# Kernel optimization log

Hardware: AMD Instinct MI355X
Metric: run time of the kernel (lower is better)

Reference implementation:

```python
import jax, jax.numpy as jnp
from jax import lax
import numpy as np

GRID = 64
HIDDEN = 256
FEAT = 128


def setup_inputs() -> dict:
    key = jax.random.key(0)
    ks = jax.random.split(key, 16)
    B, S = 1024, 4096
    def w(k, shape, fan_in):
        return (jax.random.normal(k, shape, jnp.float32) * (1.0 / np.sqrt(fan_in))).astype(jnp.float32)
    return {
        "x": jax.random.normal(ks[0], (B, 2, S), jnp.float32),
        # conv stack
        "w1": w(ks[1], (32, 1, 3, 3), 9),    "b1": jnp.zeros((32,), jnp.float32),  "a1": jnp.float32(0.25),
        "w2": w(ks[2], (64, 32, 3, 3), 32 * 9),  "b2": jnp.zeros((64,), jnp.float32),  "a2": jnp.float32(0.25),
        "w3": w(ks[3], (128, 64, 5, 5), 64 * 25), "b3": jnp.zeros((128,), jnp.float32), "a3": jnp.float32(0.25),
        # classifier (dropout is identity in eval mode)
        "wc1": w(ks[4], (HIDDEN, 128 * 4 * 4), 128 * 16), "bc1": jnp.zeros((HIDDEN,), jnp.float32), "ac": jnp.float32(0.25),
        "wc2": w(ks[5], (FEAT, HIDDEN), HIDDEN),          "bc2": jnp.zeros((FEAT,), jnp.float32),
    }


def _prelu(x, a):
    return jnp.where(x > 0, x, a * x)


def _conv(x, w, b, pad):
    y = lax.conv_general_dilated(x, w, (1, 1), [(pad, pad), (pad, pad)],
                                 dimension_numbers=("NCHW", "OIHW", "NCHW"))
    return y + b[None, :, None, None]


def _avgpool2(x):  # kernel 2, stride 2 (also serves as adaptive pool 8->4)
    B, C, H, W = x.shape
    return x.reshape(B, C, H // 2, 2, W // 2, 2).mean(axis=(3, 5))


def _iq_to_constellation(x):
    # x: [B, 2, S] -> occupancy grid [B, 1, G, G] (set to 1.0, duplicates collapse)
    B = x.shape[0]
    scale = GRID // 2 / 2.0
    offset = GRID // 2
    ii = jnp.clip((x[:, 0] * scale + offset).astype(jnp.int32), 0, GRID - 1)  # [B,S]
    qi = jnp.clip((x[:, 1] * scale + offset).astype(jnp.int32), 0, GRID - 1)
    img = jnp.zeros((B, 1, GRID, GRID), x.dtype)
    bidx = jnp.arange(B)[:, None]
    return img.at[bidx, 0, qi, ii].set(1.0)


def reference(x, w1, b1, a1, w2, b2, a2, w3, b3, a3, wc1, bc1, ac, wc2, bc2):
    img = _iq_to_constellation(x)                      # [B,1,64,64]
    h = _avgpool2(_prelu(_conv(img, w1, b1, 1), a1))   # [B,32,32,32]
    h = _avgpool2(_prelu(_conv(h, w2, b2, 1), a2))     # [B,64,16,16]
    h = _avgpool2(_prelu(_conv(h, w3, b3, 2), a3))     # [B,128,8,8]
    h = _avgpool2(h)                                   # adaptive 8x8 -> 4x4
    h = h.reshape(h.shape[0], -1)                      # [B, 2048]
    h = _prelu(h @ wc1.T + bc1, ac)                    # [B, 256]
    return h @ wc2.T + bc2                             # [B, 128]
```

## Files before the change

kernel.cpp:

```cpp
#include <hip/hip_runtime.h>


typedef short s16x8 __attribute__((ext_vector_type(8)));
typedef float f32x4 __attribute__((ext_vector_type(4)));
typedef float f32x16 __attribute__((ext_vector_type(16)));
typedef unsigned u32x4 __attribute__((ext_vector_type(4)));
typedef unsigned u32x2 __attribute__((ext_vector_type(2)));

__device__ __forceinline__ float prelu(float v, float a) {
    return v > 0.0f ? v : a * v;
}
__device__ __forceinline__ unsigned short bf16_rn(float x) {
    union { float f; unsigned u; } a; a.f = x;
    unsigned r = a.u + 0x7FFF + ((a.u >> 16) & 1);
    return (unsigned short)(r >> 16);
}
__device__ __forceinline__ unsigned pack2(float lo, float hi) {
    return (unsigned)bf16_rn(lo) | ((unsigned)bf16_rn(hi) << 16);
}

__global__ __launch_bounds__(256) void k_prepack_all(
    const float* __restrict__ w3, unsigned short* __restrict__ w3pk,
    const float* __restrict__ w2, unsigned short* __restrict__ w2pk,
    const float* __restrict__ wc1, unsigned short* __restrict__ wf1pk,
    const float* __restrict__ wc2, unsigned short* __restrict__ wf2pk)
{
    const int bid = blockIdx.x;
    const int t = threadIdx.x;
    if (bid < 800) {
        int e = bid * 256 + t;
        int i  = e & 7;
        int co = (e >> 3) & 127;
        int g  = (e >> 10) & 3;
        int kk = (e >> 12) & 1;
        int tp = e >> 13;
        int ci = kk * 32 + g * 8 + i;
        w3pk[e] = bf16_rn(w3[((size_t)co * 64 + ci) * 25 + tp]);
    } else if (bid < 872) {
        int e = (bid - 800) * 256 + t;
        int i   = e & 7;
        int l   = (e >> 3) & 63;
        int mt  = (e >> 9) & 1;
        int kkk = (e >> 10) & 1;
        int tap = e >> 11;
        int co = mt * 32 + (l & 31);
        int ci = kkk * 16 + (l >> 5) * 8 + i;
        w2pk[e] = bf16_rn(w2[((size_t)co * 32 + ci) * 9 + tap]);
    } else if (bid < 2920) {
        int e = (bid - 872) * 256 + t;
        int i   = e & 7;
        int hid = (e >> 3) & 255;
        int g   = (e >> 11) & 3;
        int kc  = e >> 13;
        int k = kc * 32 + g * 8 + i;
        wf1pk[e] = bf16_rn(wc1[(size_t)hid * 2048 + k]);
    } else {
        int e = (bid - 2920) * 256 + t;
        int i  = e & 7;
        int o  = (e >> 3) & 127;
        int g  = (e >> 10) & 3;
        int kc = e >> 12;
        int k = kc * 32 + g * 8 + i;
        wf2pk[e] = bf16_rn(wc2[(size_t)o * 256 + k]);
    }
}

__global__ __launch_bounds__(256) void k_scat_conv1(
    const float* __restrict__ x, const float* __restrict__ w1,
    const float* __restrict__ b1, const float* __restrict__ a1,
    unsigned short* __restrict__ out1, int b0)
{
    __shared__ float img[34 * 66];
    __shared__ float ws[32 * 9];
    __shared__ float bs[32];
    const int t = threadIdx.x;
    const int bl = blockIdx.x >> 1;
    const int yb = blockIdx.x & 1;
    const int b = b0 + bl;

    for (int i = t; i < 34 * 66; i += 256) img[i] = 0.0f;
    for (int i = t; i < 288; i += 256) ws[i] = w1[i];
    if (t < 32) bs[t] = b1[t];
    __syncthreads();

    const float* xb = x + (size_t)b * 8192;
    const int rbase = yb * 32 - 1;
    for (int s = t; s < 4096; s += 256) {
        float xi = xb[s];
        float xq = xb[4096 + s];
        int ii = (int)(xi * 16.0f + 32.0f);
        int qi = (int)(xq * 16.0f + 32.0f);
        ii = min(max(ii, 0), 63);
        qi = min(max(qi, 0), 63);
        int r = qi - rbase;
        if (r >= 0 && r < 34) img[r * 66 + (ii + 1)] = 1.0f;
    }
    __syncthreads();

    const float alpha = a1[0];
    unsigned short* ob = out1 + (size_t)bl * 32768;
    for (int i = 0; i < 2; ++i) {
        int p = i * 256 + t;
        int pyl = p >> 5, px = p & 31;
        float v[4][4];
        #pragma unroll
        for (int r = 0; r < 4; ++r)
            #pragma unroll
            for (int c = 0; c < 4; ++c)
                v[r][c] = img[(2 * pyl + r) * 66 + (2 * px + c)];
        const int pg = (yb * 16 + pyl) * 32 + px;
        unsigned short* dst = ob + (size_t)pg * 32;
        #pragma unroll 2
        for (int c4 = 0; c4 < 8; ++c4) {
            float o4[4];
            #pragma unroll
            for (int h = 0; h < 4; ++h) {
                const int c = c4 * 4 + h;
                float w[9];
                #pragma unroll
                for (int k = 0; k < 9; ++k) w[k] = ws[c * 9 + k];
                float s00 = 0.f, s01 = 0.f, s10 = 0.f, s11 = 0.f;
                #pragma unroll
                for (int ky = 0; ky < 3; ++ky)
                    #pragma unroll
                    for (int kx = 0; kx < 3; ++kx) {
                        float wk = w[ky * 3 + kx];
                        s00 = fmaf(v[ky][kx],         wk, s00);
                        s01 = fmaf(v[ky][kx + 1],     wk, s01);
                        s10 = fmaf(v[ky + 1][kx],     wk, s10);
                        s11 = fmaf(v[ky + 1][kx + 1], wk, s11);
                    }
                float bb = bs[c];
                o4[h] = 0.25f * (prelu(s00 + bb, alpha) + prelu(s01 + bb, alpha) +
                                 prelu(s10 + bb, alpha) + prelu(s11 + bb, alpha));
            }
            u32x2 q = {pack2(o4[0], o4[1]), pack2(o4[2], o4[3])};
            *reinterpret_cast<u32x2*>(dst + c4 * 4) = q;
        }
    }
}

__global__ __launch_bounds__(512) void k_conv2_mfma(
    const unsigned short* __restrict__ in1, const unsigned short* __restrict__ wpk,
    const float* __restrict__ b2, const float* __restrict__ a2,
    unsigned short* __restrict__ out2)
{
    __shared__ __align__(16) unsigned short lb[4 * 18 * 36 * 8];
    __shared__ float bs[64];
    const int t = threadIdx.x;
    const int bl = blockIdx.x >> 1;
    const int yb = blockIdx.x & 1;
    const int lane = t & 63;
    const int q = t >> 6;
    const int hl = lane >> 5;
    const int c31 = lane & 31;

    if (t < 64) bs[t] = b2[t];

    const s16x8 zz = {0, 0, 0, 0, 0, 0, 0, 0};
    for (int idx = t; idx < 2592; idx += 512)
        reinterpret_cast<s16x8*>(lb)[idx] = zz;
    __syncthreads();

    for (int idx = t; idx < 576; idx += 512) {
        int ly = idx >> 5;
        int xx = idx & 31;
        int y = yb * 16 + ly - 1;
        if (y >= 0 && y < 32) {
            const s16x8* src = reinterpret_cast<const s16x8*>(
                in1 + ((size_t)bl * 1024 + y * 32 + xx) * 32);
            #pragma unroll
            for (int cg = 0; cg < 4; ++cg) {
                *reinterpret_cast<s16x8*>(&lb[((cg * 18 + ly) * 36 + (xx + 1)) * 8]) = src[cg];
            }
        }
    }
    __syncthreads();

    f32x16 acc[2][2];
    #pragma unroll
    for (int m = 0; m < 2; ++m)
        #pragma unroll
        for (int n = 0; n < 2; ++n)
            #pragma unroll
            for (int e = 0; e < 16; ++e) acc[m][n][e] = 0.0f;

    #pragma unroll
    for (int kkk = 0; kkk < 2; ++kkk) {
        const int g = kkk * 2 + hl;
        #pragma unroll
        for (int dx = 0; dx < 3; ++dx) {
            const int sx = c31 + dx;
            s16x8 breg[4];
            #pragma unroll
            for (int j = 0; j < 4; ++j)
                breg[j] = *reinterpret_cast<const s16x8*>(
                    &lb[((g * 18 + 2 * q + j) * 36 + sx) * 8]);
            #pragma unroll
            for (int dy = 0; dy < 3; ++dy) {
                const int tap = dy * 3 + dx;
                const unsigned short* wb =
                    wpk + ((size_t)(tap * 2 + kkk) * 2) * 512 + lane * 8;
                s16x8 a0 = *reinterpret_cast<const s16x8*>(wb);
                s16x8 a1 = *reinterpret_cast<const s16x8*>(wb + 512);
                acc[0][0] = __builtin_amdgcn_mfma_f32_32x32x16_bf16(a0, breg[dy],     acc[0][0], 0, 0, 0);
                acc[0][1] = __builtin_amdgcn_mfma_f32_32x32x16_bf16(a0, breg[dy + 1], acc[0][1], 0, 0, 0);
                acc[1][0] = __builtin_amdgcn_mfma_f32_32x32x16_bf16(a1, breg[dy],     acc[1][0], 0, 0, 0);
                acc[1][1] = __builtin_amdgcn_mfma_f32_32x32x16_bf16(a1, breg[dy + 1], acc[1][1], 0, 0, 0);
            }
        }
    }

    const float alpha = a2[0];
    const int gy = yb * 8 + q;
    const int gx = c31 >> 1;
    #pragma unroll
    for (int mt = 0; mt < 2; ++mt) {
        float sv[16];
        #pragma unroll
        for (int r = 0; r < 16; ++r) {
            const int co = mt * 32 + (r & 3) + 8 * (r >> 2) + 4 * hl;
            const float bb = bs[co];
            float s = prelu(acc[mt][0][r] + bb, alpha) + prelu(acc[mt][1][r] + bb, alpha);
            s += __shfl_xor(s, 1, 64);
            sv[r] = s * 0.25f;
        }
        if ((lane & 1) == 0) {
            unsigned short* dst = out2 + ((size_t)bl * 256 + gy * 16 + gx) * 64;
            #pragma unroll
            for (int rp = 0; rp < 8; ++rp) {
                const int r = rp * 2;
                const int co0 = mt * 32 + (r & 3) + 8 * (r >> 2) + 4 * hl;
                *reinterpret_cast<unsigned*>(dst + co0) = pack2(sv[r], sv[r + 1]);
            }
        }
    }
}

__global__ __launch_bounds__(512) void k_conv3_mfma(
    const unsigned short* __restrict__ in2, const unsigned short* __restrict__ wpk,
    const float* __restrict__ b3, const float* __restrict__ a3,
    unsigned short* __restrict__ out3h, int b0)
{
    __shared__ __align__(16) unsigned short lb[8 * 20 * 20 * 8];
    __shared__ float bs[128];

    const int t = threadIdx.x;
    const int bl = blockIdx.x;
    const int lane = t & 63;
    const int w = t >> 6;
    const int mp = w >> 1;
    const int nh = w & 1;
    const int lg = lane >> 4;
    const int lo16 = lane & 15;

    if (t < 128) bs[t] = b3[t];

    const s16x8 zz = {0, 0, 0, 0, 0, 0, 0, 0};
    for (int idx = t; idx < 3200; idx += 512)
        reinterpret_cast<s16x8*>(lb)[idx] = zz;
    __syncthreads();

    for (int idx = t; idx < 2048; idx += 512) {
        int g = idx >> 8;
        int pix = idx & 255;
        int row = pix >> 4;
        int xx = pix & 15;
        s16x8 v = *reinterpret_cast<const s16x8*>(
            in2 + ((size_t)bl * 256 + row * 16 + xx) * 64 + g * 8);
        *reinterpret_cast<s16x8*>(&lb[((g * 20 + (row + 2)) * 20 + (xx + 2)) * 8]) = v;
    }
    __syncthreads();

    const f32x4 zf = {0.f, 0.f, 0.f, 0.f};
    f32x4 acc[2][8];
    #pragma unroll
    for (int m = 0; m < 2; ++m)
        #pragma unroll
        for (int n = 0; n < 8; ++n) acc[m][n] = zf;

    for (int kk = 0; kk < 2; ++kk) {
        const int rowbase = (kk * 4 + lg) * 20 + nh * 8;
        #pragma unroll
        for (int dx = 0; dx < 5; ++dx) {
            const int ax = lo16 + dx;
            s16x8 breg[12];
            #pragma unroll
            for (int j = 0; j < 12; ++j)
                breg[j] = *reinterpret_cast<const s16x8*>(
                    &lb[((rowbase + j) * 20 + ax) * 8]);
            #pragma unroll
            for (int dy = 0; dy < 5; ++dy) {
                const int tap = dy * 5 + dx;
                const size_t wbase = ((size_t)(tap * 2 + kk) * 4 + lg) * 1024
                                   + (size_t)(mp * 32 + lo16) * 8;
                s16x8 a0 = *reinterpret_cast<const s16x8*>(wpk + wbase);
                s16x8 a1 = *reinterpret_cast<const s16x8*>(wpk + wbase + 128);
                #pragma unroll
                for (int n = 0; n < 8; ++n) {
                    acc[0][n] = __builtin_amdgcn_mfma_f32_16x16x32_bf16(a0, breg[n + dy], acc[0][n], 0, 0, 0);
                    acc[1][n] = __builtin_amdgcn_mfma_f32_16x16x32_bf16(a1, breg[n + dy], acc[1][n], 0, 0, 0);
                }
            }
        }
    }

    const float alpha = a3[0];
    const int b = b0 + bl;
    const int fx = lo16 >> 2;
    #pragma unroll
    for (int m = 0; m < 2; ++m) {
        const int cobase = mp * 32 + m * 16 + lg * 4;
        #pragma unroll
        for (int r = 0; r < 4; ++r) {
            float bb = bs[cobase + r];
            #pragma unroll
            for (int half = 0; half < 2; ++half) {
                float s = 0.f;
                #pragma unroll
                for (int j = 0; j < 4; ++j) {
                    float v = acc[m][half * 4 + j][r] + bb;
                    s += v > 0.f ? v : alpha * v;
                }
                s += __shfl_xor(s, 1, 64);
                s += __shfl_xor(s, 2, 64);
                if ((lane & 3) == 0) {
                    int fy = nh * 2 + half;
                    out3h[(size_t)b * 2048 + (cobase + r) * 16 + fy * 4 + fx] =
                        bf16_rn(s * 0.0625f);
                }
            }
        }
    }
}

__global__ __launch_bounds__(512) void k_fc_mfma(
    const unsigned short* __restrict__ h, const unsigned short* __restrict__ w1pk,
    const float* __restrict__ bc1, const float* __restrict__ ac,
    const unsigned short* __restrict__ w2pk, const float* __restrict__ bc2,
    float* __restrict__ out)
{
    __shared__ __align__(16) unsigned short hid_lds[16][264];
    __shared__ float bs1[256];
    __shared__ float bs2[128];
    const int t = threadIdx.x;
    const int lane = t & 63;
    const int w = t >> 6;
    const int lg = lane >> 4;
    const int lo16 = lane & 15;

    if (t < 256) bs1[t] = bc1[t];
    if (t < 128) bs2[t] = bc2[t];

    const size_t rb = (size_t)blockIdx.x * 16 + lo16;

    const f32x4 zf = {0.f, 0.f, 0.f, 0.f};
    f32x4 acc1[2];
    acc1[0] = zf; acc1[1] = zf;

    const unsigned short* hrow = h + rb * 2048;
    #pragma unroll 2
    for (int kc = 0; kc < 64; ++kc) {
        s16x8 bfrag = *reinterpret_cast<const s16x8*>(hrow + kc * 32 + lg * 8);
        #pragma unroll
        for (int mt = 0; mt < 2; ++mt) {
            s16x8 afr = *reinterpret_cast<const s16x8*>(
                w1pk + ((size_t)(kc * 4 + lg) * 256 + (w * 2 + mt) * 16 + lo16) * 8);
            acc1[mt] = __builtin_amdgcn_mfma_f32_16x16x32_bf16(afr, bfrag, acc1[mt], 0, 0, 0);
        }
    }

    __syncthreads();
    const float alpha = ac[0];
    #pragma unroll
    for (int mt = 0; mt < 2; ++mt) {
        const int hid0 = (w * 2 + mt) * 16 + lg * 4;
        float v0 = prelu(acc1[mt][0] + bs1[hid0 + 0], alpha);
        float v1 = prelu(acc1[mt][1] + bs1[hid0 + 1], alpha);
        float v2 = prelu(acc1[mt][2] + bs1[hid0 + 2], alpha);
        float v3 = prelu(acc1[mt][3] + bs1[hid0 + 3], alpha);
        u32x2 q = {pack2(v0, v1), pack2(v2, v3)};
        *reinterpret_cast<u32x2*>(&hid_lds[lo16][hid0]) = q;
    }
    __syncthreads();

    f32x4 acc2 = zf;
    #pragma unroll
    for (int kc = 0; kc < 8; ++kc) {
        s16x8 bfrag = *reinterpret_cast<const s16x8*>(&hid_lds[lo16][kc * 32 + lg * 8]);
        s16x8 afr = *reinterpret_cast<const s16x8*>(
            w2pk + ((size_t)(kc * 4 + lg) * 128 + w * 16 + lo16) * 8);
        acc2 = __builtin_amdgcn_mfma_f32_16x16x32_bf16(afr, bfrag, acc2, 0, 0, 0);
    }

    const int o0 = w * 16 + lg * 4;
    #pragma unroll
    for (int r = 0; r < 4; ++r)
        out[rb * 128 + o0 + r] = acc2[r] + bs2[o0 + r];
}

extern "C" void kernel_launch(void* const* d_in, const int* in_sizes, int n_in,
                              void* d_out, int out_size, void* d_ws, size_t ws_size,
                              hipStream_t stream) {
    const float* x   = (const float*)d_in[0];
    const float* w1  = (const float*)d_in[1];
    const float* b1  = (const float*)d_in[2];
    const float* a1  = (const float*)d_in[3];
    const float* w2  = (const float*)d_in[4];
    const float* b2  = (const float*)d_in[5];
    const float* a2  = (const float*)d_in[6];
    const float* w3  = (const float*)d_in[7];
    const float* b3  = (const float*)d_in[8];
    const float* a3  = (const float*)d_in[9];
    const float* wc1 = (const float*)d_in[10];
    const float* bc1 = (const float*)d_in[11];
    const float* ac  = (const float*)d_in[12];
    const float* wc2 = (const float*)d_in[13];
    const float* bc2 = (const float*)d_in[14];
    float* out = (float*)d_out;

    const size_t OUT3_BYTES = (size_t)1024 * 2048 * 2;
    const size_t W3PK = (size_t)204800 * 2;
    const size_t W2PK = (size_t)18432 * 2;
    const size_t WFC1 = (size_t)524288 * 2;
    const size_t WFC2 = (size_t)32768 * 2;
    const size_t FIXED = OUT3_BYTES + W3PK + W2PK + WFC1 + WFC2;
    int C = 1024;
    while (C > 1 && FIXED + (size_t)C * (65536 + 32768) > ws_size) C >>= 1;

    char* p = (char*)d_ws;
    unsigned short* out3h = (unsigned short*)p;  p += OUT3_BYTES;
    unsigned short* w3pk  = (unsigned short*)p;  p += W3PK;
    unsigned short* w2pk  = (unsigned short*)p;  p += W2PK;
    unsigned short* wf1pk = (unsigned short*)p;  p += WFC1;
    unsigned short* wf2pk = (unsigned short*)p;  p += WFC2;
    unsigned short* out1  = (unsigned short*)p;  p += (size_t)C * 65536;
    unsigned short* out2  = (unsigned short*)p;

    k_prepack_all<<<3048, 256, 0, stream>>>(w3, w3pk, w2, w2pk, wc1, wf1pk, wc2, wf2pk);

    const int nchunk = 1024 / C;
    for (int c = 0; c < nchunk; ++c) {
        int b0 = c * C;
        k_scat_conv1<<<2 * C, 256, 0, stream>>>(x, w1, b1, a1, out1, b0);
        k_conv2_mfma<<<2 * C, 512, 0, stream>>>(out1, w2pk, b2, a2, out2);
        k_conv3_mfma<<<C, 512, 0, stream>>>(out2, w3pk, b3, a3, out3h, b0);
    }
    k_fc_mfma<<<64, 512, 0, stream>>>(out3h, wf1pk, bc1, ac, wf2pk, bc2, out);
}
```

Before: 238.4 us.

## Fuse weight prepack into conv1 launch and restructure conv3 to skip padded rows

The weight-prepack kernel is folded into the first chunk's scatter+conv1 launch as extra leading blocks, removing one kernel launch and letting both kinds of work overlap. conv3 drops the vertical zero padding from its LDS tile and instead skips MFMAs for out-of-range rows. It loads B fragments per tap from LDS instead of caching 12 registers per dx, and adds a launch bound with a min-blocks hint to raise occupancy. Bias now comes straight from global memory. The tradeoff is more LDS reads and branchy inner loops in exchange for fewer registers, less LDS, and skipped boundary MFMAs.

```diff
diff --git a/kernel.cpp b/kernel.cpp
--- a/kernel.cpp
+++ b/kernel.cpp
@@ -19,63 +19,63 @@
     return (unsigned)bf16_rn(lo) | ((unsigned)bf16_rn(hi) << 16);
 }
 
-__global__ __launch_bounds__(256) void k_prepack_all(
+__global__ __launch_bounds__(256) void k_front(
+    const float* __restrict__ x, const float* __restrict__ w1,
+    const float* __restrict__ b1, const float* __restrict__ a1,
+    unsigned short* __restrict__ out1, int b0, int np,
     const float* __restrict__ w3, unsigned short* __restrict__ w3pk,
     const float* __restrict__ w2, unsigned short* __restrict__ w2pk,
     const float* __restrict__ wc1, unsigned short* __restrict__ wf1pk,
     const float* __restrict__ wc2, unsigned short* __restrict__ wf2pk)
 {
-    const int bid = blockIdx.x;
     const int t = threadIdx.x;
-    if (bid < 800) {
-        int e = bid * 256 + t;
-        int i  = e & 7;
-        int co = (e >> 3) & 127;
-        int g  = (e >> 10) & 3;
-        int kk = (e >> 12) & 1;
-        int tp = e >> 13;
-        int ci = kk * 32 + g * 8 + i;
-        w3pk[e] = bf16_rn(w3[((size_t)co * 64 + ci) * 25 + tp]);
-    } else if (bid < 872) {
-        int e = (bid - 800) * 256 + t;
-        int i   = e & 7;
-        int l   = (e >> 3) & 63;
-        int mt  = (e >> 9) & 1;
-        int kkk = (e >> 10) & 1;
-        int tap = e >> 11;
-        int co = mt * 32 + (l & 31);
-        int ci = kkk * 16 + (l >> 5) * 8 + i;
-        w2pk[e] = bf16_rn(w2[((size_t)co * 32 + ci) * 9 + tap]);
-    } else if (bid < 2920) {
-        int e = (bid - 872) * 256 + t;
-        int i   = e & 7;
-        int hid = (e >> 3) & 255;
-        int g   = (e >> 11) & 3;
-        int kc  = e >> 13;
-        int k = kc * 32 + g * 8 + i;
-        wf1pk[e] = bf16_rn(wc1[(size_t)hid * 2048 + k]);
-    } else {
-        int e = (bid - 2920) * 256 + t;
-        int i  = e & 7;
-        int o  = (e >> 3) & 127;
-        int g  = (e >> 10) & 3;
-        int kc = e >> 12;
-        int k = kc * 32 + g * 8 + i;
-        wf2pk[e] = bf16_rn(wc2[(size_t)o * 256 + k]);
-    }
-}
-
-__global__ __launch_bounds__(256) void k_scat_conv1(
-    const float* __restrict__ x, const float* __restrict__ w1,
-    const float* __restrict__ b1, const float* __restrict__ a1,
-    unsigned short* __restrict__ out1, int b0)
-{
+    if ((int)blockIdx.x < np) {
+        const int bid = blockIdx.x;
+        if (bid < 800) {
+            int e = bid * 256 + t;
+            int i  = e & 7;
+            int co = (e >> 3) & 127;
+            int g  = (e >> 10) & 3;
+            int kk = (e >> 12) & 1;
+            int tp = e >> 13;
+            int ci = kk * 32 + g * 8 + i;
+            w3pk[e] = bf16_rn(w3[((size_t)co * 64 + ci) * 25 + tp]);
+        } else if (bid < 872) {
+            int e = (bid - 800) * 256 + t;
+            int i   = e & 7;
+            int l   = (e >> 3) & 63;
+            int mt  = (e >> 9) & 1;
+            int kkk = (e >> 10) & 1;
+            int tap = e >> 11;
+            int co = mt * 32 + (l & 31);
+            int ci = kkk * 16 + (l >> 5) * 8 + i;
+            w2pk[e] = bf16_rn(w2[((size_t)co * 32 + ci) * 9 + tap]);
+        } else if (bid < 2920) {
+            int e = (bid - 872) * 256 + t;
+            int i   = e & 7;
+            int hid = (e >> 3) & 255;
+            int g   = (e >> 11) & 3;
+            int kc  = e >> 13;
+            int k = kc * 32 + g * 8 + i;
+            wf1pk[e] = bf16_rn(wc1[(size_t)hid * 2048 + k]);
+        } else {
+            int e = (bid - 2920) * 256 + t;
+            int i  = e & 7;
+            int o  = (e >> 3) & 127;
+            int g  = (e >> 10) & 3;
+            int kc = e >> 12;
+            int k = kc * 32 + g * 8 + i;
+            wf2pk[e] = bf16_rn(wc2[(size_t)o * 256 + k]);
+        }
+        return;
+    }
+
     __shared__ float img[34 * 66];
     __shared__ float ws[32 * 9];
     __shared__ float bs[32];
-    const int t = threadIdx.x;
-    const int bl = blockIdx.x >> 1;
-    const int yb = blockIdx.x & 1;
+    const int cbid = blockIdx.x - np;
+    const int bl = cbid >> 1;
+    const int yb = cbid & 1;
     const int b = b0 + bl;
 
     for (int i = t; i < 34 * 66; i += 256) img[i] = 0.0f;
@@ -237,13 +237,12 @@
     }
 }
 
-__global__ __launch_bounds__(512) void k_conv3_mfma(
+__global__ __launch_bounds__(512, 8) void k_conv3_mfma(
     const unsigned short* __restrict__ in2, const unsigned short* __restrict__ wpk,
     const float* __restrict__ b3, const float* __restrict__ a3,
     unsigned short* __restrict__ out3h, int b0)
 {
-    __shared__ __align__(16) unsigned short lb[8 * 20 * 20 * 8];
-    __shared__ float bs[128];
+    __shared__ __align__(16) unsigned short lb[8 * 16 * 20 * 8];
 
     const int t = threadIdx.x;
     const int bl = blockIdx.x;
@@ -254,10 +253,8 @@
     const int lg = lane >> 4;
     const int lo16 = lane & 15;
 
-    if (t < 128) bs[t] = b3[t];
-
     const s16x8 zz = {0, 0, 0, 0, 0, 0, 0, 0};
-    for (int idx = t; idx < 3200; idx += 512)
+    for (int idx = t; idx < 2560; idx += 512)
         reinterpret_cast<s16x8*>(lb)[idx] = zz;
     __syncthreads();
 
@@ -268,7 +265,7 @@
         int xx = pix & 15;
         s16x8 v = *reinterpret_cast<const s16x8*>(
             in2 + ((size_t)bl * 256 + row * 16 + xx) * 64 + g * 8);
-        *reinterpret_cast<s16x8*>(&lb[((g * 20 + (row + 2)) * 20 + (xx + 2)) * 8]) = v;
+        *reinterpret_cast<s16x8*>(&lb[((g * 16 + row) * 20 + (xx + 2)) * 8]) = v;
     }
     __syncthreads();
 
@@ -280,26 +277,20 @@
         for (int n = 0; n < 8; ++n) acc[m][n] = zf;
 
     for (int kk = 0; kk < 2; ++kk) {
-        const int rowbase = (kk * 4 + lg) * 20 + nh * 8;
-        #pragma unroll
-        for (int dx = 0; dx < 5; ++dx) {
-            const int ax = lo16 + dx;
-            s16x8 breg[12];
-            #pragma unroll
-            for (int j = 0; j < 12; ++j)
-                breg[j] = *reinterpret_cast<const s16x8*>(
-                    &lb[((rowbase + j) * 20 + ax) * 8]);
-            #pragma unroll
-            for (int dy = 0; dy < 5; ++dy) {
-                const int tap = dy * 5 + dx;
-                const size_t wbase = ((size_t)(tap * 2 + kk) * 4 + lg) * 1024
-                                   + (size_t)(mp * 32 + lo16) * 8;
-                s16x8 a0 = *reinterpret_cast<const s16x8*>(wpk + wbase);
-                s16x8 a1 = *reinterpret_cast<const s16x8*>(wpk + wbase + 128);
-                #pragma unroll
-                for (int n = 0; n < 8; ++n) {
-                    acc[0][n] = __builtin_amdgcn_mfma_f32_16x16x32_bf16(a0, breg[n + dy], acc[0][n], 0, 0, 0);
-                    acc[1][n] = __builtin_amdgcn_mfma_f32_16x16x32_bf16(a1, breg[n + dy], acc[1][n], 0, 0, 0);
+        for (int tap = 0; tap < 25; ++tap) {
+            int dy = tap / 5, dx = tap - dy * 5;
+            const size_t wbase = ((size_t)(tap * 2 + kk) * 4 + lg) * 1024
+                               + (size_t)(mp * 32 + lo16) * 8;
+            s16x8 a0 = *reinterpret_cast<const s16x8*>(wpk + wbase);
+            s16x8 a1 = *reinterpret_cast<const s16x8*>(wpk + wbase + 128);
+            #pragma unroll
+            for (int n = 0; n < 8; ++n) {
+                const int row = nh * 8 + n + dy - 2;
+                if (row >= 0 && row < 16) {
+                    s16x8 bfrag = *reinterpret_cast<const s16x8*>(
+                        &lb[(((kk * 4 + lg) * 16 + row) * 20 + lo16 + dx) * 8]);
+                    acc[0][n] = __builtin_amdgcn_mfma_f32_16x16x32_bf16(a0, bfrag, acc[0][n], 0, 0, 0);
+                    acc[1][n] = __builtin_amdgcn_mfma_f32_16x16x32_bf16(a1, bfrag, acc[1][n], 0, 0, 0);
                 }
             }
         }
@@ -313,7 +304,7 @@
         const int cobase = mp * 32 + m * 16 + lg * 4;
         #pragma unroll
         for (int r = 0; r < 4; ++r) {
-            float bb = bs[cobase + r];
+            float bb = b3[cobase + r];
             #pragma unroll
             for (int half = 0; half < 2; ++half) {
                 float s = 0.f;
@@ -437,12 +428,13 @@
     unsigned short* out1  = (unsigned short*)p;  p += (size_t)C * 65536;
     unsigned short* out2  = (unsigned short*)p;
 
-    k_prepack_all<<<3048, 256, 0, stream>>>(w3, w3pk, w2, w2pk, wc1, wf1pk, wc2, wf2pk);
-
     const int nchunk = 1024 / C;
     for (int c = 0; c < nchunk; ++c) {
         int b0 = c * C;
-        k_scat_conv1<<<2 * C, 256, 0, stream>>>(x, w1, b1, a1, out1, b0);
+        int np = (c == 0) ? 3048 : 0;
+        k_front<<<np + 2 * C, 256, 0, stream>>>(
+            x, w1, b1, a1, out1, b0, np,
+            w3, w3pk, w2, w2pk, wc1, wf1pk, wc2, wf2pk);
         k_conv2_mfma<<<2 * C, 512, 0, stream>>>(out1, w2pk, b2, a2, out2);
         k_conv3_mfma<<<C, 512, 0, stream>>>(out2, w3pk, b3, a3, out3h, b0);
     }
```

Result: slower. 825.7 us (+246.4%).
